# Performance work log

Hardware: AMD Instinct MI355X
Metric: run time of the kernel (lower is better)

## Reference

```python
import jax, jax.numpy as jnp
import numpy as np

HEADS = 8

def setup_inputs() -> dict:
    key = jax.random.key(0)
    ks = jax.random.split(key, 5)
    B, C, H, W = 2, 256, 64, 64
    dim = C
    x = jax.random.normal(ks[0], (B, C, H, W), dtype=jnp.float32)
    # Linear weights stored as [in, out] so y = x @ W + b
    w_qkv = jax.random.normal(ks[1], (dim, 3 * dim), dtype=jnp.float32) * (dim ** -0.5)
    b_qkv = jax.random.normal(ks[2], (3 * dim,), dtype=jnp.float32) * 0.02
    w_out = jax.random.normal(ks[3], (dim, dim), dtype=jnp.float32) * (dim ** -0.5)
    b_out = jax.random.normal(ks[4], (dim,), dtype=jnp.float32) * 0.02
    return {"x": x, "w_qkv": w_qkv, "b_qkv": b_qkv, "w_out": w_out, "b_out": b_out}

def reference(x, w_qkv, b_qkv, w_out, b_out):
    B, C, H, W = x.shape
    h = HEADS
    d = C // h
    scale = d ** -0.5
    # [B, C, H, W] -> [B, N, C]
    tokens = x.reshape(B, C, H * W).transpose(0, 2, 1)
    qkv = tokens @ w_qkv + b_qkv  # [B, N, 3C]
    q, k, v = jnp.split(qkv, 3, axis=-1)
    def to_heads(t):
        Bn, N, _ = t.shape
        return t.reshape(Bn, N, h, d).transpose(0, 2, 1, 3)  # [B, h, N, d]
    q, k, v = map(to_heads, (q, k, v))
    dots = jnp.einsum('bhnd,bhmd->bhnm', q, k) * scale  # [B, h, N, N]
    attn = jax.nn.softmax(dots, axis=-1)
    out = jnp.einsum('bhnm,bhmd->bhnd', attn, v)  # [B, h, N, d]
    out = out.transpose(0, 2, 1, 3).reshape(B, H * W, C)  # [B, N, C]
    out = out @ w_out + b_out
    return out.transpose(0, 2, 1).reshape(B, C, H, W)
```

## Files before the change

### kernel.cpp

```cpp
#include <hip/hip_runtime.h>

typedef __attribute__((ext_vector_type(8))) short s16x8;
typedef __attribute__((ext_vector_type(4))) short s16x4;
typedef __attribute__((ext_vector_type(4))) float f32x4;
typedef __attribute__((ext_vector_type(2))) unsigned u32x2;

#define MFMA32(a, b, c) __builtin_amdgcn_mfma_f32_16x16x32_bf16((a), (b), (c), 0, 0, 0)

#if __has_builtin(__builtin_amdgcn_mfma_f32_16x16x16bf16_1k)
#define MFMA16K(a, b, c) __builtin_amdgcn_mfma_f32_16x16x16bf16_1k((a), (b), (c), 0, 0, 0)
#else
#define MFMA16K(a, b, c) (c)
#endif

#if __has_builtin(__builtin_amdgcn_exp2f)
#define EXP2F(x) __builtin_amdgcn_exp2f(x)
#else
#define EXP2F(x) __exp2f(x)
#endif

#if __has_builtin(__builtin_amdgcn_rcpf)
#define RCPF(x) __builtin_amdgcn_rcpf(x)
#else
#define RCPF(x) (1.0f / (x))
#endif

#define SL2E 0.25507313f

__device__ __forceinline__ unsigned pkrne(float a, float b) {
  unsigned ua = __builtin_bit_cast(unsigned, a);
  unsigned ub = __builtin_bit_cast(unsigned, b);
  ua += 0x7FFFu + ((ua >> 16) & 1u);
  ub += 0x7FFFu + ((ub >> 16) & 1u);
  return __builtin_amdgcn_perm(ub, ua, 0x07060302u);
}

__device__ __forceinline__ unsigned pktrunc(float a, float b) {
  return __builtin_amdgcn_perm(__builtin_bit_cast(unsigned, b),
                               __builtin_bit_cast(unsigned, a), 0x07060302u);
}

__device__ __forceinline__ unsigned short bfr(float f) {
  unsigned u = __builtin_bit_cast(unsigned, f);
  u += 0x7FFFu + ((u >> 16) & 1u);
  return (unsigned short)(u >> 16);
}

__device__ __forceinline__ float bflo(unsigned u) {
  return __builtin_bit_cast(float, u << 16);
}
__device__ __forceinline__ float bfhi(unsigned u) {
  return __builtin_bit_cast(float, u & 0xFFFF0000u);
}

__global__ __launch_bounds__(256) void prep_kernel(
    const float* __restrict__ x, const float* __restrict__ wqkv,
    const float* __restrict__ wout, ushort* __restrict__ xbf,
    ushort* __restrict__ wT, ushort* __restrict__ woT) {
  const int t = threadIdx.x;
  const int sub = t & 15, grp = t >> 4;
  const int id = blockIdx.x;
  const float* src;
  ushort* dst;
  int src_ld, k0, n0;
  float sc = 1.f;
  if (id < 512) {
    int mt = id & 63, kt = (id >> 6) & 3, b = id >> 8;
    src = x + (size_t)b * 256 * 4096;
    src_ld = 4096;
    dst = xbf + (size_t)b * 4096 * 256;
    k0 = kt * 64;
    n0 = mt * 64;
  } else if (id < 560) {
    int r = id - 512, nt = r % 12, kt = r / 12;
    src = wqkv;
    src_ld = 768;
    dst = wT;
    k0 = kt * 64;
    n0 = nt * 64;
    if (n0 < 256) sc = SL2E;
  } else {
    int r = id - 560, nt = r & 3, kt = r >> 2;
    src = wout;
    src_ld = 256;
    dst = woT;
    k0 = kt * 64;
    n0 = nt * 64;
  }
  const int k = k0 + grp * 4;
  const int n = n0 + sub * 4;
  unsigned d0[4], d1[4];
#pragma unroll
  for (int i = 0; i < 4; ++i) {
    float4 v = *(const float4*)(src + (size_t)(k + i) * src_ld + n);
    d0[i] = pkrne(v.x * sc, v.y * sc);
    d1[i] = pkrne(v.z * sc, v.w * sc);
  }
  u32x2 r0 = {__builtin_amdgcn_perm(d0[1], d0[0], 0x05040100u),
              __builtin_amdgcn_perm(d0[3], d0[2], 0x05040100u)};
  u32x2 r1 = {__builtin_amdgcn_perm(d0[1], d0[0], 0x07060302u),
              __builtin_amdgcn_perm(d0[3], d0[2], 0x07060302u)};
  u32x2 r2 = {__builtin_amdgcn_perm(d1[1], d1[0], 0x05040100u),
              __builtin_amdgcn_perm(d1[3], d1[2], 0x05040100u)};
  u32x2 r3 = {__builtin_amdgcn_perm(d1[1], d1[0], 0x07060302u),
              __builtin_amdgcn_perm(d1[3], d1[2], 0x07060302u)};
  *(u32x2*)(dst + (size_t)(n + 0) * 256 + k) = r0;
  *(u32x2*)(dst + (size_t)(n + 1) * 256 + k) = r1;
  *(u32x2*)(dst + (size_t)(n + 2) * 256 + k) = r2;
  *(u32x2*)(dst + (size_t)(n + 3) * 256 + k) = r3;
}

__global__ __launch_bounds__(256) void qkv_kernel(
    const ushort* __restrict__ xbf, const ushort* __restrict__ wT,
    const float* __restrict__ bq, ushort* __restrict__ QG,
    ushort* __restrict__ KG, ushort* __restrict__ VtG) {
  __shared__ __align__(16) ushort Wl[64][40];
  __shared__ __align__(16) ushort Xl[128][40];
  const int t0 = blockIdx.x * 128;
  const int n0 = blockIdx.y * 64;
  const int t = threadIdx.x;
  const int wid = t >> 6, lane = t & 63;
  const int wy = wid >> 1, wx = wid & 1;
  const int quad = lane >> 4, l16 = lane & 15;
  f32x4 acc[2][4] = {};
  const int wr = t >> 2, wsg = t & 3;
  for (int k0 = 0; k0 < 256; k0 += 32) {
    __syncthreads();
    *(uint4*)&Wl[wr][wsg * 8] =
        *(const uint4*)(wT + (size_t)(n0 + wr) * 256 + k0 + wsg * 8);
#pragma unroll
    for (int i = 0; i < 2; ++i) {
      int fid = t + 256 * i, row = fid >> 2, seg = fid & 3;
      *(uint4*)&Xl[row][seg * 8] =
          *(const uint4*)(xbf + (size_t)(t0 + row) * 256 + k0 + seg * 8);
    }
    __syncthreads();
    s16x8 wf[2], xf[4];
#pragma unroll
    for (int i = 0; i < 2; ++i)
      wf[i] = *(const s16x8*)&Wl[32 * wy + 16 * i + l16][quad * 8];
#pragma unroll
    for (int j = 0; j < 4; ++j)
      xf[j] = *(const s16x8*)&Xl[64 * wx + 16 * j + l16][quad * 8];
#pragma unroll
    for (int i = 0; i < 2; ++i)
#pragma unroll
      for (int j = 0; j < 4; ++j) acc[i][j] = MFMA32(wf[i], xf[j], acc[i][j]);
  }
  if (n0 < 512) {
    ushort* dst = (n0 < 256) ? QG : KG;
    const float bsc = (n0 < 256) ? SL2E : 1.f;
#pragma unroll
    for (int i = 0; i < 2; ++i) {
      int nb = n0 + 32 * wy + 16 * i + 4 * quad;
      float4 b4 = *(const float4*)(bq + nb);
      float bx0 = b4.x * bsc, bx1 = b4.y * bsc, bx2 = b4.z * bsc,
            bx3 = b4.w * bsc;
      int h = ((nb & 255) >> 5);
      int dd0 = nb & 31;
#pragma unroll
      for (int j = 0; j < 4; ++j) {
        int tok = t0 + 64 * wx + 16 * j + l16;
        int b = tok >> 12, tokn = tok & 4095;
        u32x2 pk = {pkrne(acc[i][j][0] + bx0, acc[i][j][1] + bx1),
                    pkrne(acc[i][j][2] + bx2, acc[i][j][3] + bx3)};
        *(u32x2*)(dst + ((size_t)(b * 8 + h) * 4096 + tokn) * 32 + dd0) = pk;
      }
    }
  } else {
#pragma unroll
    for (int i = 0; i < 2; ++i) {
      int nb = n0 + 32 * wy + 16 * i + 4 * quad;
      float4 b4 = *(const float4*)(bq + nb);
      float bb[4] = {b4.x, b4.y, b4.z, b4.w};
#pragma unroll
      for (int r = 0; r < 4; ++r) {
        int nn = nb + r - 512;
        int h = nn >> 5, ddv = nn & 31;
        ushort* vrow = VtG + (size_t)(h * 32 + ddv) * 4096;
#pragma unroll
        for (int j = 0; j < 4; ++j) {
          int tok = t0 + 64 * wx + 16 * j + l16;
          int b = tok >> 12, tokn = tok & 4095;
          vrow[(size_t)b * 8 * 32 * 4096 + tokn] = bfr(acc[i][j][r] + bb[r]);
        }
      }
    }
  }
}

__global__ __launch_bounds__(256, 6) void attn_split(
    const ushort* __restrict__ QG, const ushort* __restrict__ KG,
    const ushort* __restrict__ VtG, ushort* __restrict__ OF0,
    ushort* __restrict__ OFb, float* __restrict__ LF) {
  __shared__ __align__(16) ushort Kl[2][64][40];
  __shared__ __align__(16) ushort Vl[2][32][72];
  const int id = blockIdx.x;
  const int bh = (id & 7) * 2 + ((id >> 3) & 1);
  const int q0 = ((id >> 4) & 31) * 128;
  const int sp = id >> 9;
  const int kt0 = (sp * 64 + 2) / 3;
  const int niter = ((sp + 1) * 64 + 2) / 3 - kt0;
  const int t = threadIdx.x;
  const int wid = t >> 6, lane = t & 63;
  const int quad = lane >> 4, l16 = lane & 15;
  const size_t base = (size_t)bh * 4096 * 32;
  const ushort* qp = QG + base;
  const ushort* kp = KG + base;
  const ushort* vp = VtG + base;
  const int qw = q0 + 32 * wid;
  const s16x8 qf0 = *(const s16x8*)(qp + (size_t)(qw + l16) * 32 + quad * 8);
  const s16x8 qf1 = *(const s16x8*)(qp + (size_t)(qw + 16 + l16) * 32 + quad * 8);
  const int kr = t >> 2, ks = t & 3;
  const int vr = t >> 3, vsg = t & 7;
  *(uint4*)&Kl[0][kr][ks * 8] =
      *(const uint4*)(kp + (size_t)(kt0 * 64 + kr) * 32 + ks * 8);
  *(uint4*)&Vl[0][vr][vsg * 8] =
      *(const uint4*)(vp + (size_t)vr * 4096 + kt0 * 64 + vsg * 8);
  const ushort* kpre = kp + (size_t)((kt0 + 1) * 64 + kr) * 32 + ks * 8;
  const ushort* vpre = vp + (size_t)vr * 4096 + (kt0 + 1) * 64 + vsg * 8;
  __syncthreads();
  f32x4 o00 = {}, o01 = {}, o10 = {}, o11 = {}, ol0 = {}, ol1 = {};
  const f32x4 zero = {};
  const s16x4 ones = {(short)0x3F80, (short)0x3F80, (short)0x3F80,
                      (short)0x3F80};
  for (int i = 0; i < niter; ++i) {
    const int cur = i & 1;
    const bool more = (i + 1) < niter;
    uint4 kv, vv;
    if (more) {
      kv = *(const uint4*)kpre;
      vv = *(const uint4*)vpre;
      kpre += 2048;
      vpre += 64;
    }
    unsigned pl0[4], ph0[4], pl1[4], ph1[4];
#pragma unroll
    for (int nb = 0; nb < 4; ++nb) {
      s16x8 kf = *(const s16x8*)&Kl[cur][16 * nb + l16][quad * 8];
      f32x4 s0 = MFMA32(kf, qf0, zero);
      f32x4 s1 = MFMA32(kf, qf1, zero);
      pl0[nb] = pktrunc(EXP2F(s0[0]), EXP2F(s0[1]));
      ph0[nb] = pktrunc(EXP2F(s0[2]), EXP2F(s0[3]));
      pl1[nb] = pktrunc(EXP2F(s1[0]), EXP2F(s1[1]));
      ph1[nb] = pktrunc(EXP2F(s1[2]), EXP2F(s1[3]));
    }
#pragma unroll
    for (int nb = 0; nb < 4; ++nb) {
      u32x2 pu0 = {pl0[nb], ph0[nb]};
      u32x2 pu1 = {pl1[nb], ph1[nb]};
      s16x4 pv0 = __builtin_bit_cast(s16x4, pu0);
      s16x4 pv1 = __builtin_bit_cast(s16x4, pu1);
      s16x4 va = *(const s16x4*)&Vl[cur][l16][16 * nb + quad * 4];
      s16x4 vb = *(const s16x4*)&Vl[cur][16 + l16][16 * nb + quad * 4];
      o00 = MFMA16K(va, pv0, o00);
      o01 = MFMA16K(vb, pv0, o01);
      o10 = MFMA16K(va, pv1, o10);
      o11 = MFMA16K(vb, pv1, o11);
      ol0 = MFMA16K(ones, pv0, ol0);
      ol1 = MFMA16K(ones, pv1, ol1);
    }
    if (more) {
      *(uint4*)&Kl[cur ^ 1][kr][ks * 8] = kv;
      *(uint4*)&Vl[cur ^ 1][vr][vsg * 8] = vv;
    }
    __syncthreads();
  }
  ushort* OFs = (sp == 0) ? OF0 : OFb + (size_t)(sp - 1) * 2097152;
  float* LFs = LF + (size_t)sp * 65536;
  const int tok0 = qw + l16;
  const size_t ob0 = ((size_t)bh * 4096 + tok0) * 32;
  const size_t ob1 = ob0 + (size_t)16 * 32;
  u32x2 w00 = {pkrne(o00[0], o00[1]), pkrne(o00[2], o00[3])};
  u32x2 w01 = {pkrne(o01[0], o01[1]), pkrne(o01[2], o01[3])};
  u32x2 w10 = {pkrne(o10[0], o10[1]), pkrne(o10[2], o10[3])};
  u32x2 w11 = {pkrne(o11[0], o11[1]), pkrne(o11[2], o11[3])};
  *(u32x2*)(OFs + ob0 + 4 * quad) = w00;
  *(u32x2*)(OFs + ob0 + 16 + 4 * quad) = w01;
  *(u32x2*)(OFs + ob1 + 4 * quad) = w10;
  *(u32x2*)(OFs + ob1 + 16 + 4 * quad) = w11;
  if (quad == 0) {
    LFs[(size_t)bh * 4096 + tok0] = ol0[0];
    LFs[(size_t)bh * 4096 + tok0 + 16] = ol1[0];
  }
}

__global__ __launch_bounds__(256) void proj_split(
    const ushort* __restrict__ OF0, const ushort* __restrict__ OFb,
    const float* __restrict__ LF, const ushort* __restrict__ woT,
    const float* __restrict__ bo, float* __restrict__ out) {
  __shared__ __align__(16) ushort Wl[64][40];
  __shared__ __align__(16) ushort Xl[128][40];
  const int t0 = blockIdx.x * 128;
  const int c0 = blockIdx.y * 64;
  const int t = threadIdx.x;
  const int wid = t >> 6, lane = t & 63;
  const int wy = wid >> 1, wx = wid & 1;
  const int quad = lane >> 4, l16 = lane & 15;
  f32x4 acc[2][4] = {};
  const int wr = t >> 2, wsg = t & 3;
  const int c8 = (t & 7) * 4;
  for (int k0 = 0; k0 < 256; k0 += 32) {
    __syncthreads();
    *(uint4*)&Wl[wr][wsg * 8] =
        *(const uint4*)(woT + (size_t)(c0 + wr) * 256 + k0 + wsg * 8);
    const int hh = k0 >> 5;
#pragma unroll
    for (int p = 0; p < 4; ++p) {
      int row = 32 * p + (t >> 3);
      int tok = t0 + row, bb = tok >> 12, tokn = tok & 4095;
      size_t ro = (size_t)(bb * 8 + hh) * 4096 + tokn;
      size_t oi = ro * 32 + c8;
      uint2 a0 = *(const uint2*)(OF0 + oi);
      uint2 a1 = *(const uint2*)(OFb + oi);
      uint2 a2 = *(const uint2*)(OFb + 2097152 + oi);
      float l = LF[ro] + LF[65536 + ro] + LF[131072 + ro];
      float inv = RCPF(l);
      f32x4 s;
      s[0] = bflo(a0.x) + bflo(a1.x) + bflo(a2.x);
      s[1] = bfhi(a0.x) + bfhi(a1.x) + bfhi(a2.x);
      s[2] = bflo(a0.y) + bflo(a1.y) + bflo(a2.y);
      s[3] = bfhi(a0.y) + bfhi(a1.y) + bfhi(a2.y);
      s *= inv;
      u32x2 pk = {pkrne(s[0], s[1]), pkrne(s[2], s[3])};
      *(u32x2*)&Xl[row][c8] = pk;
    }
    __syncthreads();
    s16x8 wf[2], xf[4];
#pragma unroll
    for (int i = 0; i < 2; ++i)
      wf[i] = *(const s16x8*)&Wl[32 * wy + 16 * i + l16][quad * 8];
#pragma unroll
    for (int j = 0; j < 4; ++j)
      xf[j] = *(const s16x8*)&Xl[64 * wx + 16 * j + l16][quad * 8];
#pragma unroll
    for (int i = 0; i < 2; ++i)
#pragma unroll
      for (int j = 0; j < 4; ++j) acc[i][j] = MFMA32(wf[i], xf[j], acc[i][j]);
  }
#pragma unroll
  for (int i = 0; i < 2; ++i) {
    int cb = c0 + 32 * wy + 16 * i + 4 * quad;
    float4 b4 = *(const float4*)(bo + cb);
    float bb[4] = {b4.x, b4.y, b4.z, b4.w};
#pragma unroll
    for (int j = 0; j < 4; ++j) {
      int tok = t0 + 64 * wx + 16 * j + l16;
      int b = tok >> 12, tokn = tok & 4095;
#pragma unroll
      for (int r = 0; r < 4; ++r)
        out[((size_t)(b * 256 + cb + r)) * 4096 + tokn] = acc[i][j][r] + bb[r];
    }
  }
}

extern "C" void kernel_launch(void* const* d_in, const int* in_sizes, int n_in,
                              void* d_out, int out_size, void* d_ws, size_t ws_size,
                              hipStream_t stream) {
  (void)in_sizes; (void)n_in; (void)out_size; (void)ws_size;
  const float* x = (const float*)d_in[0];
  const float* wq = (const float*)d_in[1];
  const float* bq = (const float*)d_in[2];
  const float* wo = (const float*)d_in[3];
  const float* bo = (const float*)d_in[4];
  float* out = (float*)d_out;
  ushort* ws = (ushort*)d_ws;
  ushort* xbf = ws;
  ushort* OF0 = ws;
  ushort* QG  = ws + 2097152;
  ushort* KG  = ws + 4194304;
  ushort* VtG = ws + 6291456;
  ushort* wT  = ws + 8388608;
  ushort* woT = ws + 8585216;
  ushort* OFb = ws + 8650752;
  float* LF = (float*)(ws + 12845056);
  prep_kernel<<<576, 256, 0, stream>>>(x, wq, wo, xbf, wT, woT);
  qkv_kernel<<<dim3(64, 12), 256, 0, stream>>>(xbf, wT, bq, QG, KG, VtG);
  attn_split<<<1536, 256, 0, stream>>>(QG, KG, VtG, OF0, OFb, LF);
  proj_split<<<dim3(64, 4), 256, 0, stream>>>(OF0, OFb, LF, woT, bo, out);
}
```

Baseline: 141.5 us.

## Double attention query tile per block and use four KV splits

Each attention block now handles 256 queries (64 per wave) instead of 128, so every K/V tile staged in LDS is reused across twice as many queries. The KV range is split four ways with 16 iterations each, where it was previously split three ways, and the grid shrinks to 1024 blocks. The projection kernel now sums four partial outputs and row-sums. Launch bounds fall to 4 waves per SIMD to fit the larger register accumulators, trading occupancy and extra partial-output traffic for fewer LDS loads per MFMA.

```diff
diff --git a/kernel.cpp b/kernel.cpp
--- a/kernel.cpp
+++ b/kernel.cpp
@@ -189,7 +189,7 @@
   }
 }
 
-__global__ __launch_bounds__(256, 6) void attn_split(
+__global__ __launch_bounds__(256, 4) void attn_split(
     const ushort* __restrict__ QG, const ushort* __restrict__ KG,
     const ushort* __restrict__ VtG, ushort* __restrict__ OF0,
     ushort* __restrict__ OFb, float* __restrict__ LF) {
@@ -197,10 +197,9 @@
   __shared__ __align__(16) ushort Vl[2][32][72];
   const int id = blockIdx.x;
   const int bh = (id & 7) * 2 + ((id >> 3) & 1);
-  const int q0 = ((id >> 4) & 31) * 128;
-  const int sp = id >> 9;
-  const int kt0 = (sp * 64 + 2) / 3;
-  const int niter = ((sp + 1) * 64 + 2) / 3 - kt0;
+  const int q0 = ((id >> 4) & 15) * 256;
+  const int sp = id >> 8;
+  const int kt0 = sp * 16;
   const int t = threadIdx.x;
   const int wid = t >> 6, lane = t & 63;
   const int quad = lane >> 4, l16 = lane & 15;
@@ -208,9 +207,11 @@
   const ushort* qp = QG + base;
   const ushort* kp = KG + base;
   const ushort* vp = VtG + base;
-  const int qw = q0 + 32 * wid;
-  const s16x8 qf0 = *(const s16x8*)(qp + (size_t)(qw + l16) * 32 + quad * 8);
-  const s16x8 qf1 = *(const s16x8*)(qp + (size_t)(qw + 16 + l16) * 32 + quad * 8);
+  const int qw = q0 + 64 * wid;
+  s16x8 qf[4];
+#pragma unroll
+  for (int f = 0; f < 4; ++f)
+    qf[f] = *(const s16x8*)(qp + (size_t)(qw + 16 * f + l16) * 32 + quad * 8);
   const int kr = t >> 2, ks = t & 3;
   const int vr = t >> 3, vsg = t & 7;
   *(uint4*)&Kl[0][kr][ks * 8] =
@@ -220,13 +221,19 @@
   const ushort* kpre = kp + (size_t)((kt0 + 1) * 64 + kr) * 32 + ks * 8;
   const ushort* vpre = vp + (size_t)vr * 4096 + (kt0 + 1) * 64 + vsg * 8;
   __syncthreads();
-  f32x4 o00 = {}, o01 = {}, o10 = {}, o11 = {}, ol0 = {}, ol1 = {};
+  f32x4 oA[4], oB[4], ol[4];
+#pragma unroll
+  for (int f = 0; f < 4; ++f) {
+    oA[f] = f32x4{};
+    oB[f] = f32x4{};
+    ol[f] = f32x4{};
+  }
   const f32x4 zero = {};
   const s16x4 ones = {(short)0x3F80, (short)0x3F80, (short)0x3F80,
                       (short)0x3F80};
-  for (int i = 0; i < niter; ++i) {
+  for (int i = 0; i < 16; ++i) {
     const int cur = i & 1;
-    const bool more = (i + 1) < niter;
+    const bool more = (i + 1) < 16;
     uint4 kv, vv;
     if (more) {
       kv = *(const uint4*)kpre;
@@ -234,31 +241,21 @@
       kpre += 2048;
       vpre += 64;
     }
-    unsigned pl0[4], ph0[4], pl1[4], ph1[4];
 #pragma unroll
     for (int nb = 0; nb < 4; ++nb) {
       s16x8 kf = *(const s16x8*)&Kl[cur][16 * nb + l16][quad * 8];
-      f32x4 s0 = MFMA32(kf, qf0, zero);
-      f32x4 s1 = MFMA32(kf, qf1, zero);
-      pl0[nb] = pktrunc(EXP2F(s0[0]), EXP2F(s0[1]));
-      ph0[nb] = pktrunc(EXP2F(s0[2]), EXP2F(s0[3]));
-      pl1[nb] = pktrunc(EXP2F(s1[0]), EXP2F(s1[1]));
-      ph1[nb] = pktrunc(EXP2F(s1[2]), EXP2F(s1[3]));
-    }
-#pragma unroll
-    for (int nb = 0; nb < 4; ++nb) {
-      u32x2 pu0 = {pl0[nb], ph0[nb]};
-      u32x2 pu1 = {pl1[nb], ph1[nb]};
-      s16x4 pv0 = __builtin_bit_cast(s16x4, pu0);
-      s16x4 pv1 = __builtin_bit_cast(s16x4, pu1);
       s16x4 va = *(const s16x4*)&Vl[cur][l16][16 * nb + quad * 4];
       s16x4 vb = *(const s16x4*)&Vl[cur][16 + l16][16 * nb + quad * 4];
-      o00 = MFMA16K(va, pv0, o00);
-      o01 = MFMA16K(vb, pv0, o01);
-      o10 = MFMA16K(va, pv1, o10);
-      o11 = MFMA16K(vb, pv1, o11);
-      ol0 = MFMA16K(ones, pv0, ol0);
-      ol1 = MFMA16K(ones, pv1, ol1);
+#pragma unroll
+      for (int f = 0; f < 4; ++f) {
+        f32x4 s = MFMA32(kf, qf[f], zero);
+        u32x2 pu = {pktrunc(EXP2F(s[0]), EXP2F(s[1])),
+                    pktrunc(EXP2F(s[2]), EXP2F(s[3]))};
+        s16x4 pv = __builtin_bit_cast(s16x4, pu);
+        oA[f] = MFMA16K(va, pv, oA[f]);
+        oB[f] = MFMA16K(vb, pv, oB[f]);
+        ol[f] = MFMA16K(ones, pv, ol[f]);
+      }
     }
     if (more) {
       *(uint4*)&Kl[cur ^ 1][kr][ks * 8] = kv;
@@ -268,20 +265,15 @@
   }
   ushort* OFs = (sp == 0) ? OF0 : OFb + (size_t)(sp - 1) * 2097152;
   float* LFs = LF + (size_t)sp * 65536;
-  const int tok0 = qw + l16;
-  const size_t ob0 = ((size_t)bh * 4096 + tok0) * 32;
-  const size_t ob1 = ob0 + (size_t)16 * 32;
-  u32x2 w00 = {pkrne(o00[0], o00[1]), pkrne(o00[2], o00[3])};
-  u32x2 w01 = {pkrne(o01[0], o01[1]), pkrne(o01[2], o01[3])};
-  u32x2 w10 = {pkrne(o10[0], o10[1]), pkrne(o10[2], o10[3])};
-  u32x2 w11 = {pkrne(o11[0], o11[1]), pkrne(o11[2], o11[3])};
-  *(u32x2*)(OFs + ob0 + 4 * quad) = w00;
-  *(u32x2*)(OFs + ob0 + 16 + 4 * quad) = w01;
-  *(u32x2*)(OFs + ob1 + 4 * quad) = w10;
-  *(u32x2*)(OFs + ob1 + 16 + 4 * quad) = w11;
-  if (quad == 0) {
-    LFs[(size_t)bh * 4096 + tok0] = ol0[0];
-    LFs[(size_t)bh * 4096 + tok0 + 16] = ol1[0];
+#pragma unroll
+  for (int f = 0; f < 4; ++f) {
+    const int tok = qw + 16 * f + l16;
+    const size_t ob = ((size_t)bh * 4096 + tok) * 32;
+    u32x2 wA = {pkrne(oA[f][0], oA[f][1]), pkrne(oA[f][2], oA[f][3])};
+    u32x2 wB = {pkrne(oB[f][0], oB[f][1]), pkrne(oB[f][2], oB[f][3])};
+    *(u32x2*)(OFs + ob + 4 * quad) = wA;
+    *(u32x2*)(OFs + ob + 16 + 4 * quad) = wB;
+    if (quad == 0) LFs[(size_t)bh * 4096 + tok] = ol[f][0];
   }
 }
 
@@ -314,13 +306,14 @@
       uint2 a0 = *(const uint2*)(OF0 + oi);
       uint2 a1 = *(const uint2*)(OFb + oi);
       uint2 a2 = *(const uint2*)(OFb + 2097152 + oi);
-      float l = LF[ro] + LF[65536 + ro] + LF[131072 + ro];
+      uint2 a3 = *(const uint2*)(OFb + 4194304 + oi);
+      float l = (LF[ro] + LF[65536 + ro]) + (LF[131072 + ro] + LF[196608 + ro]);
       float inv = RCPF(l);
       f32x4 s;
-      s[0] = bflo(a0.x) + bflo(a1.x) + bflo(a2.x);
-      s[1] = bfhi(a0.x) + bfhi(a1.x) + bfhi(a2.x);
-      s[2] = bflo(a0.y) + bflo(a1.y) + bflo(a2.y);
-      s[3] = bfhi(a0.y) + bfhi(a1.y) + bfhi(a2.y);
+      s[0] = (bflo(a0.x) + bflo(a1.x)) + (bflo(a2.x) + bflo(a3.x));
+      s[1] = (bfhi(a0.x) + bfhi(a1.x)) + (bfhi(a2.x) + bfhi(a3.x));
+      s[2] = (bflo(a0.y) + bflo(a1.y)) + (bflo(a2.y) + bflo(a3.y));
+      s[3] = (bfhi(a0.y) + bfhi(a1.y)) + (bfhi(a2.y) + bfhi(a3.y));
       s *= inv;
       u32x2 pk = {pkrne(s[0], s[1]), pkrne(s[2], s[3])};
       *(u32x2*)&Xl[row][c8] = pk;
@@ -373,9 +366,9 @@
   ushort* wT  = ws + 8388608;
   ushort* woT = ws + 8585216;
   ushort* OFb = ws + 8650752;
-  float* LF = (float*)(ws + 12845056);
+  float* LF = (float*)(ws + 14942208);
   prep_kernel<<<576, 256, 0, stream>>>(x, wq, wo, xbf, wT, woT);
   qkv_kernel<<<dim3(64, 12), 256, 0, stream>>>(xbf, wT, bq, QG, KG, VtG);
-  attn_split<<<1536, 256, 0, stream>>>(QG, KG, VtG, OF0, OFb, LF);
+  attn_split<<<1024, 256, 0, stream>>>(QG, KG, VtG, OF0, OFb, LF);
   proj_split<<<dim3(64, 4), 256, 0, stream>>>(OF0, OFb, LF, woT, bo, out);
 }
```

Measured after the change: 142.9 us. Within noise of the previous version (+1.0%).
